# Kernel optimization log

Hardware: AMD Instinct MI355X
Metric: run time of the kernel (lower is better)

## Reference

```python
import jax, jax.numpy as jnp
import numpy as np

B, C, H, W = 512, 3, 32, 32
N = 50000
D = C * H * W  # 3072


def setup_inputs() -> dict:
    key = jax.random.key(0)
    k1, k2, k3 = jax.random.split(key, 3)
    x = jax.random.normal(k1, (B, C, H, W), dtype=jnp.float32)
    # per-sample noise levels, strictly positive
    sigma = jax.random.uniform(k2, (B,), dtype=jnp.float32, minval=0.5, maxval=2.0)
    # reference dataset, normalized images in [-1, 1], flattened to (N, D)
    y = jax.random.uniform(k3, (N, D), dtype=jnp.float32, minval=-1.0, maxval=1.0)
    return {"x": x, "sigma": sigma, "y": y}


def reference(x, sigma, y):
    Bb, Cc, Hh, Ww = x.shape
    xf = x.astype(jnp.float32).reshape(Bb, Cc * Hh * Ww)          # (B, D)
    s = sigma.astype(jnp.float32).reshape(-1, 1)                  # (B, 1)
    # squared euclidean distance via the GEMM expansion (matches cdist(p=2)**2)
    x2 = jnp.sum(xf * xf, axis=1, keepdims=True)                  # (B, 1)
    y2 = jnp.sum(y * y, axis=1)[None, :]                          # (1, N)
    d2 = jnp.maximum(x2 + y2 - 2.0 * (xf @ y.T), 0.0)             # (B, N)
    logits = -d2 / (2.0 * s * s)                                  # (B, N)
    prob = jax.nn.softmax(logits, axis=1)                         # (B, N)
    denoised = prob @ y                                           # (B, D)
    return denoised.reshape(Bb, Cc, Hh, Ww)
```

## Files before the change

### kernel.cpp

```cpp
#include <hip/hip_runtime.h>


typedef __attribute__((ext_vector_type(4))) float f32x4;
typedef __attribute__((ext_vector_type(4))) int i32x4;
typedef __attribute__((ext_vector_type(4))) char c8x4;
typedef __attribute__((ext_vector_type(16))) char c8x16;
typedef __attribute__((ext_vector_type(4))) unsigned short u16x4;
typedef __attribute__((ext_vector_type(8))) unsigned short u16x8;
typedef __attribute__((ext_vector_type(8))) __bf16 bf16x8;

#define NREAL 50000
#define NP    50176
#define DD    3072
#define BB    512

#define WAIT0  asm volatile("s_waitcnt vmcnt(0)" ::: "memory")
#define VM2    asm volatile("s_waitcnt vmcnt(2)" ::: "memory")
#define VM6    asm volatile("s_waitcnt vmcnt(6)" ::: "memory")
#define VM10   asm volatile("s_waitcnt vmcnt(10)" ::: "memory")
#define LGKM0  asm volatile("s_waitcnt lgkmcnt(0)" ::: "memory")
#define BAR    __builtin_amdgcn_s_barrier()
#define SCHED0 __builtin_amdgcn_sched_barrier(0)

#define SX (6.0f / 127.0f)
#define SY (1.0f / 127.0f)

__device__ __forceinline__ unsigned short f32_bf16_rne(float f) {
  unsigned int u = __float_as_uint(f);
  unsigned int r = 0x7FFFu + ((u >> 16) & 1u);
  return (unsigned short)((u + r) >> 16);
}
__device__ __forceinline__ void gload16(const void* g, void* l) {
  __builtin_amdgcn_global_load_lds(
      (const __attribute__((address_space(1))) void*)g,
      (__attribute__((address_space(3))) void*)l, 16, 0, 0);
}
__device__ __forceinline__ bf16x8 ldsldb(const unsigned short* p) {
  return __builtin_bit_cast(bf16x8, *(const u16x8*)p);
}
__device__ __forceinline__ i32x4 ldsld4(const char* p) {
  return *(const i32x4*)p;
}
__device__ __forceinline__ char q8(float f, float sc) {
  float an = rintf(f * sc);
  an = fminf(127.f, fmaxf(-127.f, an));
  return (char)(int)an;
}

__global__ __launch_bounds__(256) void zero_kernel(f32x4* p) {
  p[(size_t)blockIdx.x * 256 + threadIdx.x] = (f32x4){0.f, 0.f, 0.f, 0.f};
}

__global__ __launch_bounds__(256) void init_kernel(int* rowmin, float* rowsum) {
  const int i = blockIdx.x * 256 + threadIdx.x;
  if (i < BB) { rowmin[i] = 0x7F800000; rowsum[i] = 0.f; }
}

__global__ __launch_bounds__(256) void prep_x_kernel(
    const float* __restrict__ x, const float* __restrict__ sigma,
    char* __restrict__ ax, char* __restrict__ bx,
    float* __restrict__ x2, float* __restrict__ inv2s2) {
  const int b = blockIdx.x, t = threadIdx.x;
  const f32x4* xr = (const f32x4*)(x + (size_t)b * DD);
  float ssq = 0.f;
#pragma unroll
  for (int i = 0; i < 3; ++i) {
    const int idx = i * 256 + t;
    f32x4 v = xr[idx];
    c8x4 a, bb;
#pragma unroll
    for (int j = 0; j < 4; ++j) {
      float f = v[j];
      ssq += f * f;
      char av = q8(f, 127.0f / 6.0f);
      a[j] = av;
      float r = f - (float)(int)av * SX;
      bb[j] = q8(r, 254.0f * 127.0f / 6.0f);
    }
    *(c8x4*)(ax + (size_t)b * DD + idx * 4) = a;
    *(c8x4*)(bx + (size_t)b * DD + idx * 4) = bb;
  }
  __shared__ float red[4];
#pragma unroll
  for (int off = 32; off > 0; off >>= 1) ssq += __shfl_xor(ssq, off);
  if ((t & 63) == 0) red[t >> 6] = ssq;
  __syncthreads();
  if (t == 0) {
    x2[b] = red[0] + red[1] + red[2] + red[3];
    float s = sigma[b];
    inv2s2[b] = 1.0f / (2.0f * s * s);
  }
}

__global__ __launch_bounds__(256) void quant_y_kernel(
    const float* __restrict__ y, char* __restrict__ ay, char* __restrict__ by,
    float* __restrict__ y2) {
  const int n = blockIdx.x, t = threadIdx.x;
  if (n >= NREAL) {
    c8x4 z = {0, 0, 0, 0};
#pragma unroll
    for (int i = 0; i < 3; ++i) {
      const int idx = i * 256 + t;
      *(c8x4*)(ay + (size_t)n * DD + idx * 4) = z;
      *(c8x4*)(by + (size_t)n * DD + idx * 4) = z;
    }
    if (t == 0) y2[n] = 0.f;
    return;
  }
  const f32x4* yr = (const f32x4*)(y + (size_t)n * DD);
  float ssq = 0.f;
#pragma unroll
  for (int i = 0; i < 3; ++i) {
    const int idx = i * 256 + t;
    f32x4 v = yr[idx];
    c8x4 a, bb;
#pragma unroll
    for (int j = 0; j < 4; ++j) {
      float f = v[j];
      ssq += f * f;
      char av = q8(f, 127.0f);
      a[j] = av;
      float r2 = f - (float)(int)av * SY;
      bb[j] = q8(r2, 254.0f * 127.0f);
    }
    *(c8x4*)(ay + (size_t)n * DD + idx * 4) = a;
    *(c8x4*)(by + (size_t)n * DD + idx * 4) = bb;
  }
  __shared__ float red[4];
#pragma unroll
  for (int off = 32; off > 0; off >>= 1) ssq += __shfl_xor(ssq, off);
  if ((t & 63) == 0) red[t >> 6] = ssq;
  __syncthreads();
  if (t == 0) y2[n] = red[0] + red[1] + red[2] + red[3];
}

__global__ __launch_bounds__(256) void tr_y_kernel(
    const char* __restrict__ ay, const char* __restrict__ by,
    unsigned short* __restrict__ yT) {
  const int bn = blockIdx.x % 784, bd = blockIdx.x / 784;
  const int n0 = bn * 64, d0 = bd * 64;
  __shared__ unsigned short T[64][66];
  const int t = threadIdx.x;
  const int r = t >> 2, cc = (t & 3) * 16;
  c8x16 a = *(const c8x16*)(ay + (size_t)(n0 + r) * DD + d0 + cc);
  c8x16 b = *(const c8x16*)(by + (size_t)(n0 + r) * DD + d0 + cc);
#pragma unroll
  for (int j = 0; j < 16; ++j) {
    float f = (float)((int)a[j] * 254 + (int)b[j]) * (SY / 254.0f);
    T[r][cc + j] = f32_bf16_rne(f);
  }
  __syncthreads();
  const int dr = t >> 2;
#pragma unroll
  for (int k = 0; k < 2; ++k) {
    const int nb = ((t & 3) * 2 + k) * 8;
    u16x8 o;
#pragma unroll
    for (int j = 0; j < 8; ++j) o[j] = T[nb + j][dr];
    *(u16x8*)(yT + (size_t)(d0 + dr) * NP + n0 + nb) = o;
  }
}

__global__ __launch_bounds__(512, 2) void qk_kernel(
    const char* __restrict__ ay, const char* __restrict__ by,
    const char* __restrict__ ax, const char* __restrict__ bx,
    const float* __restrict__ x2, const float* __restrict__ inv2s2,
    const float* __restrict__ y2, float* __restrict__ S, int* __restrict__ rowmin) {
  const int orig = blockIdx.x;
  const int virt = (orig & 7) * 98 + (orig >> 3);
  const int mt = virt & 1, nt = virt >> 1;
  const int m0 = mt * 256, n0 = nt * 128;
  const int t = threadIdx.x, lane = t & 63, w = t >> 6;
  const int wm = w >> 1, wn = w & 1;
  const int l15 = lane & 15;
  const int cs = ((lane >> 4) ^ ((l15 >> 1) & 3)) * 16;

  __shared__ __align__(16) char L[3][49152];

  i32x4 acc1[4][4] = {};
  i32x4 acc2[4][4] = {};

  const int srow = t >> 2;
  const int sc = ((t & 3) ^ ((t >> 3) & 3)) * 16;
  const int sdst = t * 16;

  const char* pax0 = ax + (size_t)(m0 + srow) * DD + sc;
  const char* pax1 = ax + (size_t)(m0 + srow + 128) * DD + sc;
  const char* pbx0 = bx + (size_t)(m0 + srow) * DD + sc;
  const char* pbx1 = bx + (size_t)(m0 + srow + 128) * DD + sc;
  const char* pay = ay + (size_t)(n0 + srow) * DD + sc;
  const char* pby = by + (size_t)(n0 + srow) * DD + sc;

  auto SA = [&](int buf) {
    char* base = L[buf];
    gload16(pax0, base + sdst);
    gload16(pax1, base + 8192 + sdst);
    gload16(pbx0, base + 16384 + sdst);
    gload16(pbx1, base + 16384 + 8192 + sdst);
    pax0 += 64; pax1 += 64; pbx0 += 64; pbx1 += 64;
  };
  auto SB = [&](int buf) {
    char* base = L[buf];
    gload16(pay, base + 32768 + sdst);
    gload16(pby, base + 40960 + sdst);
    pay += 64; pby += 64;
  };

  i32x4 ayf[4], byf[4], axf[2], bxf[2];
  auto RB = [&](int buf) {
    const char* base = L[buf];
#pragma unroll
    for (int nf = 0; nf < 4; ++nf) {
      const int row = wn * 64 + nf * 16 + l15;
      ayf[nf] = ldsld4(base + 32768 + row * 64 + cs);
      byf[nf] = ldsld4(base + 40960 + row * 64 + cs);
    }
  };
  auto RA = [&](int buf, int mh) {
    const char* base = L[buf];
#pragma unroll
    for (int m2 = 0; m2 < 2; ++m2) {
      const int row = wm * 64 + (mh * 2 + m2) * 16 + l15;
      axf[m2] = ldsld4(base + row * 64 + cs);
      bxf[m2] = ldsld4(base + 16384 + row * 64 + cs);
    }
  };
  auto MF = [&](int mh) {
    __builtin_amdgcn_s_setprio(1);
#pragma unroll
    for (int m2 = 0; m2 < 2; ++m2) {
      const int mf = mh * 2 + m2;
#pragma unroll
      for (int nf = 0; nf < 4; ++nf) {
        acc1[mf][nf] = __builtin_amdgcn_mfma_i32_16x16x64_i8(axf[m2], ayf[nf], acc1[mf][nf], 0, 0, 0);
        acc2[mf][nf] = __builtin_amdgcn_mfma_i32_16x16x64_i8(axf[m2], byf[nf], acc2[mf][nf], 0, 0, 0);
        acc2[mf][nf] = __builtin_amdgcn_mfma_i32_16x16x64_i8(bxf[m2], ayf[nf], acc2[mf][nf], 0, 0, 0);
      }
    }
    __builtin_amdgcn_s_setprio(0);
  };

  SA(0); SB(0); SA(1); SB(1);

  for (int k = 0; k < 48; ++k) {
    const int buf = k % 3;
    BAR;
    if (k <= 45) SA((k + 2) % 3);
    if (k <= 45) { VM10; } else if (k == 46) { VM6; } else { WAIT0; }
    BAR;
    RB(buf); RA(buf, 0);
    MF(0);
    if (k <= 45) SB((k + 2) % 3);
    RA(buf, 1);
    MF(1);
  }

  const float C1 = 6.0f / 16129.0f;
  const float C2 = C1 / 254.0f;
  float rmv[4][4];
#pragma unroll
  for (int mf = 0; mf < 4; ++mf)
#pragma unroll
    for (int i = 0; i < 4; ++i) rmv[mf][i] = 3.0e38f;

#pragma unroll
  for (int nf = 0; nf < 4; ++nf) {
    const int col = n0 + wn * 64 + nf * 16 + l15;
    const bool ok = (col < NREAL);
    const float yy = ok ? y2[col] : 0.f;
#pragma unroll
    for (int mf = 0; mf < 4; ++mf) {
#pragma unroll
      for (int i = 0; i < 4; ++i) {
        const int row = m0 + wm * 64 + mf * 16 + ((lane >> 4) * 4) + i;
        float v = 3.0e38f;
        if (ok) {
          float dot = C1 * (float)acc1[mf][nf][i] + C2 * (float)acc2[mf][nf][i];
          float d2 = fmaxf(x2[row] + yy - 2.0f * dot, 0.0f);
          v = d2 * inv2s2[row];
          rmv[mf][i] = fminf(rmv[mf][i], v);
        }
        S[(size_t)row * NP + col] = v;
      }
    }
  }
#pragma unroll
  for (int mf = 0; mf < 4; ++mf)
#pragma unroll
    for (int i = 0; i < 4; ++i) {
      float v = rmv[mf][i];
#pragma unroll
      for (int o = 1; o < 16; o <<= 1) v = fminf(v, __shfl_xor(v, o));
      rmv[mf][i] = v;
    }
  if (l15 == 0) {
#pragma unroll
    for (int mf = 0; mf < 4; ++mf)
#pragma unroll
      for (int i = 0; i < 4; ++i) {
        const int row = m0 + wm * 64 + mf * 16 + ((lane >> 4) * 4) + i;
        atomicMin(rowmin + row, __float_as_int(rmv[mf][i]));
      }
  }
}

__global__ __launch_bounds__(256) void softmax_kernel(
    const float* __restrict__ S, const int* __restrict__ rowmin,
    unsigned short* __restrict__ P, float* __restrict__ rowsum) {
  const int bid = blockIdx.x;
  const int b = bid / 7, c = bid % 7;
  const int t = threadIdx.x;
  const f32x4* row = (const f32x4*)(S + (size_t)b * NP);
  const float rm = __int_as_float(rowmin[b]);
  unsigned short* pr = P + (size_t)b * NP;
  float sum = 0.f;
  const int base = c * 1792;
#pragma unroll
  for (int i = 0; i < 7; ++i) {
    const int e = base + i * 256 + t;
    f32x4 v = row[e];
    float e0 = __expf(rm - v[0]), e1 = __expf(rm - v[1]);
    float e2 = __expf(rm - v[2]), e3 = __expf(rm - v[3]);
    sum += e0 + e1 + e2 + e3;
    u16x4 o;
    o[0] = f32_bf16_rne(e0); o[1] = f32_bf16_rne(e1);
    o[2] = f32_bf16_rne(e2); o[3] = f32_bf16_rne(e3);
    *(u16x4*)(pr + (size_t)e * 4) = o;
  }
#pragma unroll
  for (int off = 32; off > 0; off >>= 1) sum += __shfl_xor(sum, off);
  __shared__ float red[4];
  if ((t & 63) == 0) red[t >> 6] = sum;
  __syncthreads();
  if (t == 0) atomicAdd(rowsum + b, red[0] + red[1] + red[2] + red[3]);
}

__global__ __launch_bounds__(512, 2) void pv_kernel(
    const unsigned short* __restrict__ yT, const unsigned short* __restrict__ P,
    const float* __restrict__ rowsum, float* __restrict__ out) {
  const int orig = blockIdx.x;
  const int virt = (orig & 7) * 96 + (orig >> 3);
  const int sp = virt / 24;
  const int r24 = virt % 24;
  const int dt = r24 >> 1, mt = r24 & 1;
  const int m0 = mt * 256, d0 = dt * 256;
  const int k0t = sp * 24 + (sp < 16 ? sp : 16);
  const int NT = 24 + (sp < 16 ? 1 : 0);

  const int t = threadIdx.x;
  const int lane = t & 63, w = t >> 6;
  const int wm = w >> 2, wn = w & 3;
  const int l15 = lane & 15;
  const int h3 = (l15 >> 1) & 7;
  const int cs0 = ((lane >> 4) ^ h3) * 8;
  const int cs1 = ((4 + (lane >> 4)) ^ h3) * 8;

  __shared__ __align__(16) unsigned short L[2][2][16384];

  f32x4 acc[8][4] = {};

  const int srow8 = t >> 3;
  const int sc = ((t & 7) ^ ((t >> 4) & 7)) * 8;
  const int sdst = t * 8;

  const size_t kbeg = (size_t)k0t * 64;
  const unsigned short* pA[4];
  pA[0] = P + (size_t)(m0 + srow8) * NP + kbeg + sc;
  pA[1] = P + (size_t)(m0 + srow8 + 128) * NP + kbeg + sc;
  pA[2] = P + (size_t)(m0 + srow8 + 64) * NP + kbeg + sc;
  pA[3] = P + (size_t)(m0 + srow8 + 192) * NP + kbeg + sc;
  const unsigned short* pB[4];
#pragma unroll
  for (int r = 0; r < 4; ++r)
    pB[r] = yT + (size_t)(d0 + srow8 + r * 64) * NP + kbeg + sc;

  auto SB01 = [&](int b) {
    gload16(pB[0], &L[b][1][sdst]); gload16(pB[1], &L[b][1][sdst + 4096]);
    pB[0] += 64; pB[1] += 64;
  };
  auto SB23 = [&](int b) {
    gload16(pB[2], &L[b][1][sdst + 8192]); gload16(pB[3], &L[b][1][sdst + 12288]);
    pB[2] += 64; pB[3] += 64;
  };
  auto SA01 = [&](int b) {
    gload16(pA[0], &L[b][0][sdst]); gload16(pA[1], &L[b][0][sdst + 4096]);
    pA[0] += 64; pA[1] += 64;
  };
  auto SA23 = [&](int b) {
    gload16(pA[2], &L[b][0][sdst + 8192]); gload16(pA[3], &L[b][0][sdst + 12288]);
    pA[2] += 64; pA[3] += 64;
  };

  bf16x8 a[4], bv[4];
  auto RA = [&](int b, int mh, int cs) {
#pragma unroll
    for (int m4 = 0; m4 < 4; ++m4)
      a[m4] = ldsldb(&L[b][0][(mh * 128 + wm * 64 + m4 * 16 + l15) * 64 + cs]);
  };
  auto RB = [&](int b, int cs) {
#pragma unroll
    for (int nf = 0; nf < 4; ++nf)
      bv[nf] = ldsldb(&L[b][1][(wn * 64 + nf * 16 + l15) * 64 + cs]);
  };
  auto MF = [&](int mh) {
    __builtin_amdgcn_s_setprio(1);
#pragma unroll
    for (int m4 = 0; m4 < 4; ++m4)
#pragma unroll
      for (int nf = 0; nf < 4; ++nf)
        acc[mh * 4 + m4][nf] = __builtin_amdgcn_mfma_f32_16x16x32_bf16(
            a[m4], bv[nf], acc[mh * 4 + m4][nf], 0, 0, 0);
    __builtin_amdgcn_s_setprio(0);
  };

  SB01(0); SB23(0); SA01(0); SA23(0);
  WAIT0; BAR;

  for (int k = 0; k < NT - 1; ++k) {
    const int b = k & 1, nb = b ^ 1;
    RB(b, cs0); RA(b, 0, cs0);
    SB01(nb);
    BAR; LGKM0; SCHED0;
    MF(0);
    VM2;
    BAR;
    RA(b, 1, cs0);
    SB23(nb);
    BAR; LGKM0; SCHED0;
    MF(1);
    BAR;
    RB(b, cs1); RA(b, 0, cs1);
    SA01(nb);
    BAR; LGKM0; SCHED0;
    MF(0);
    BAR;
    RA(b, 1, cs1);
    SA23(nb);
    BAR; LGKM0; SCHED0;
    MF(1);
    VM2;
    BAR;
  }
  {
    const int b = (NT - 1) & 1;
    RB(b, cs0); RA(b, 0, cs0);
    BAR; LGKM0; SCHED0;
    MF(0);
    WAIT0;
    BAR;
    RA(b, 1, cs0);
    LGKM0; SCHED0;
    MF(1);
    RB(b, cs1); RA(b, 0, cs1);
    LGKM0; SCHED0;
    MF(0);
    RA(b, 1, cs1);
    LGKM0; SCHED0;
    MF(1);
  }

#pragma unroll
  for (int mi = 0; mi < 8; ++mi)
#pragma unroll
    for (int i = 0; i < 4; ++i) {
      const int row = m0 + wm * 128 + mi * 16 + ((lane >> 4) * 4) + i;
      const float scale = 1.0f / rowsum[row];
#pragma unroll
      for (int nf = 0; nf < 4; ++nf) {
        const int col = d0 + wn * 64 + nf * 16 + l15;
        unsafeAtomicAdd(out + (size_t)row * DD + col, acc[mi][nf][i] * scale);
      }
    }
}

extern "C" void kernel_launch(void* const* d_in, const int* in_sizes, int n_in,
                              void* d_out, int out_size, void* d_ws, size_t ws_size,
                              hipStream_t stream) {
  const float* x = (const float*)d_in[0];
  const float* sigma = (const float*)d_in[1];
  const float* y = (const float*)d_in[2];
  float* out = (float*)d_out;
  char* ws = (char*)d_ws;

  size_t off = 0;
  float* S = (float*)(ws + off);                      off += (size_t)BB * NP * 4;
  char* ay = (char*)(ws + off);                       off += (size_t)NP * DD;
  char* by = (char*)(ws + off);                       off += (size_t)NP * DD;
  unsigned short* P = (unsigned short*)by;
  char* ax = (char*)(ws + off);                       off += (size_t)BB * DD;
  char* bx = (char*)(ws + off);                       off += (size_t)BB * DD;
  float* y2 = (float*)(ws + off);                     off += (size_t)NP * 4;
  float* x2 = (float*)(ws + off);                     off += 512 * 4;
  float* inv2s2 = (float*)(ws + off);                 off += 512 * 4;
  float* rowsum = (float*)(ws + off);                 off += 512 * 4;
  int* rowmin = (int*)(ws + off);                     off += 512 * 4;
  unsigned short* yT = (unsigned short*)(ws + off);   off += (size_t)DD * NP * 2;
  off += 65536;
  if (ws_size < off) return;

  zero_kernel<<<dim3(1536), dim3(256), 0, stream>>>((f32x4*)out);
  init_kernel<<<dim3(2), dim3(256), 0, stream>>>(rowmin, rowsum);
  prep_x_kernel<<<dim3(512), dim3(256), 0, stream>>>(x, sigma, ax, bx, x2, inv2s2);
  quant_y_kernel<<<dim3(NP), dim3(256), 0, stream>>>(y, ay, by, y2);
  tr_y_kernel<<<dim3(784 * 48), dim3(256), 0, stream>>>(ay, by, yT);
  qk_kernel<<<dim3(784), dim3(512), 0, stream>>>(ay, by, ax, bx, x2, inv2s2, y2, S, rowmin);
  softmax_kernel<<<dim3(512 * 7), dim3(256), 0, stream>>>(S, rowmin, P, rowsum);
  pv_kernel<<<dim3(768), dim3(512), 0, stream>>>(yT, P, rowsum, out);
}
```

Before: 931.4 us.

## Shrink QK GEMM tiles to 128x128 with single-buffered LDS staging

The int8 distance GEMM now uses 256-thread blocks computing 128x128 output tiles, so twice as many blocks are launched. The triple-buffered, barrier-interleaved global→LDS pipeline is replaced by one 32KB buffer filled between two __syncthreads per k-step. The intent is to cut LDS use and raise occupancy and block count. In exchange, load latency no longer overlaps with MFMA work, and operand reuse per byte loaded drops.

```diff
diff --git a/kernel.cpp b/kernel.cpp
--- a/kernel.cpp
+++ b/kernel.cpp
@@ -16,8 +16,6 @@
 
 #define WAIT0  asm volatile("s_waitcnt vmcnt(0)" ::: "memory")
 #define VM2    asm volatile("s_waitcnt vmcnt(2)" ::: "memory")
-#define VM6    asm volatile("s_waitcnt vmcnt(6)" ::: "memory")
-#define VM10   asm volatile("s_waitcnt vmcnt(10)" ::: "memory")
 #define LGKM0  asm volatile("s_waitcnt lgkmcnt(0)" ::: "memory")
 #define BAR    __builtin_amdgcn_s_barrier()
 #define SCHED0 __builtin_amdgcn_sched_barrier(0)
@@ -161,21 +159,21 @@
   }
 }
 
-__global__ __launch_bounds__(512, 2) void qk_kernel(
+__global__ __launch_bounds__(256, 2) void qk_kernel(
     const char* __restrict__ ay, const char* __restrict__ by,
     const char* __restrict__ ax, const char* __restrict__ bx,
     const float* __restrict__ x2, const float* __restrict__ inv2s2,
     const float* __restrict__ y2, float* __restrict__ S, int* __restrict__ rowmin) {
   const int orig = blockIdx.x;
-  const int virt = (orig & 7) * 98 + (orig >> 3);
-  const int mt = virt & 1, nt = virt >> 1;
-  const int m0 = mt * 256, n0 = nt * 128;
+  const int virt = (orig & 7) * 196 + (orig >> 3);
+  const int mt = virt & 3, nt = virt >> 2;
+  const int m0 = mt * 128, n0 = nt * 128;
   const int t = threadIdx.x, lane = t & 63, w = t >> 6;
   const int wm = w >> 1, wn = w & 1;
   const int l15 = lane & 15;
   const int cs = ((lane >> 4) ^ ((l15 >> 1) & 3)) * 16;
 
-  __shared__ __align__(16) char L[3][49152];
+  __shared__ __align__(16) char L[32768];
 
   i32x4 acc1[4][4] = {};
   i32x4 acc2[4][4] = {};
@@ -185,74 +183,58 @@
   const int sdst = t * 16;
 
   const char* pax0 = ax + (size_t)(m0 + srow) * DD + sc;
-  const char* pax1 = ax + (size_t)(m0 + srow + 128) * DD + sc;
+  const char* pax1 = ax + (size_t)(m0 + srow + 64) * DD + sc;
   const char* pbx0 = bx + (size_t)(m0 + srow) * DD + sc;
-  const char* pbx1 = bx + (size_t)(m0 + srow + 128) * DD + sc;
-  const char* pay = ay + (size_t)(n0 + srow) * DD + sc;
-  const char* pby = by + (size_t)(n0 + srow) * DD + sc;
-
-  auto SA = [&](int buf) {
-    char* base = L[buf];
-    gload16(pax0, base + sdst);
-    gload16(pax1, base + 8192 + sdst);
-    gload16(pbx0, base + 16384 + sdst);
-    gload16(pbx1, base + 16384 + 8192 + sdst);
+  const char* pbx1 = bx + (size_t)(m0 + srow + 64) * DD + sc;
+  const char* pay0 = ay + (size_t)(n0 + srow) * DD + sc;
+  const char* pay1 = ay + (size_t)(n0 + srow + 64) * DD + sc;
+  const char* pby0 = by + (size_t)(n0 + srow) * DD + sc;
+  const char* pby1 = by + (size_t)(n0 + srow + 64) * DD + sc;
+
+  auto STAGE = [&]() {
+    gload16(pax0, L + sdst);
+    gload16(pax1, L + 4096 + sdst);
+    gload16(pbx0, L + 8192 + sdst);
+    gload16(pbx1, L + 12288 + sdst);
+    gload16(pay0, L + 16384 + sdst);
+    gload16(pay1, L + 20480 + sdst);
+    gload16(pby0, L + 24576 + sdst);
+    gload16(pby1, L + 28672 + sdst);
     pax0 += 64; pax1 += 64; pbx0 += 64; pbx1 += 64;
-  };
-  auto SB = [&](int buf) {
-    char* base = L[buf];
-    gload16(pay, base + 32768 + sdst);
-    gload16(pby, base + 40960 + sdst);
-    pay += 64; pby += 64;
-  };
-
-  i32x4 ayf[4], byf[4], axf[2], bxf[2];
-  auto RB = [&](int buf) {
-    const char* base = L[buf];
+    pay0 += 64; pay1 += 64; pby0 += 64; pby1 += 64;
+  };
+  auto COMPUTE = [&]() {
+    i32x4 axf[4], bxf[4], ayf[4], byf[4];
 #pragma unroll
     for (int nf = 0; nf < 4; ++nf) {
       const int row = wn * 64 + nf * 16 + l15;
-      ayf[nf] = ldsld4(base + 32768 + row * 64 + cs);
-      byf[nf] = ldsld4(base + 40960 + row * 64 + cs);
-    }
-  };
-  auto RA = [&](int buf, int mh) {
-    const char* base = L[buf];
-#pragma unroll
-    for (int m2 = 0; m2 < 2; ++m2) {
-      const int row = wm * 64 + (mh * 2 + m2) * 16 + l15;
-      axf[m2] = ldsld4(base + row * 64 + cs);
-      bxf[m2] = ldsld4(base + 16384 + row * 64 + cs);
-    }
-  };
-  auto MF = [&](int mh) {
+      ayf[nf] = ldsld4(L + 16384 + row * 64 + cs);
+      byf[nf] = ldsld4(L + 24576 + row * 64 + cs);
+    }
+#pragma unroll
+    for (int mf = 0; mf < 4; ++mf) {
+      const int row = wm * 64 + mf * 16 + l15;
+      axf[mf] = ldsld4(L + row * 64 + cs);
+      bxf[mf] = ldsld4(L + 8192 + row * 64 + cs);
+    }
     __builtin_amdgcn_s_setprio(1);
 #pragma unroll
-    for (int m2 = 0; m2 < 2; ++m2) {
-      const int mf = mh * 2 + m2;
+    for (int mf = 0; mf < 4; ++mf)
 #pragma unroll
       for (int nf = 0; nf < 4; ++nf) {
-        acc1[mf][nf] = __builtin_amdgcn_mfma_i32_16x16x64_i8(axf[m2], ayf[nf], acc1[mf][nf], 0, 0, 0);
-        acc2[mf][nf] = __builtin_amdgcn_mfma_i32_16x16x64_i8(axf[m2], byf[nf], acc2[mf][nf], 0, 0, 0);
-        acc2[mf][nf] = __builtin_amdgcn_mfma_i32_16x16x64_i8(bxf[m2], ayf[nf], acc2[mf][nf], 0, 0, 0);
+        acc1[mf][nf] = __builtin_amdgcn_mfma_i32_16x16x64_i8(axf[mf], ayf[nf], acc1[mf][nf], 0, 0, 0);
+        acc2[mf][nf] = __builtin_amdgcn_mfma_i32_16x16x64_i8(axf[mf], byf[nf], acc2[mf][nf], 0, 0, 0);
+        acc2[mf][nf] = __builtin_amdgcn_mfma_i32_16x16x64_i8(bxf[mf], ayf[nf], acc2[mf][nf], 0, 0, 0);
       }
-    }
     __builtin_amdgcn_s_setprio(0);
   };
 
-  SA(0); SB(0); SA(1); SB(1);
-
+  STAGE();
   for (int k = 0; k < 48; ++k) {
-    const int buf = k % 3;
-    BAR;
-    if (k <= 45) SA((k + 2) % 3);
-    if (k <= 45) { VM10; } else if (k == 46) { VM6; } else { WAIT0; }
-    BAR;
-    RB(buf); RA(buf, 0);
-    MF(0);
-    if (k <= 45) SB((k + 2) % 3);
-    RA(buf, 1);
-    MF(1);
+    __syncthreads();
+    COMPUTE();
+    __syncthreads();
+    if (k < 47) STAGE();
   }
 
   const float C1 = 6.0f / 16129.0f;
@@ -503,7 +485,7 @@
   prep_x_kernel<<<dim3(512), dim3(256), 0, stream>>>(x, sigma, ax, bx, x2, inv2s2);
   quant_y_kernel<<<dim3(NP), dim3(256), 0, stream>>>(y, ay, by, y2);
   tr_y_kernel<<<dim3(784 * 48), dim3(256), 0, stream>>>(ay, by, yT);
-  qk_kernel<<<dim3(784), dim3(512), 0, stream>>>(ay, by, ax, bx, x2, inv2s2, y2, S, rowmin);
+  qk_kernel<<<dim3(1568), dim3(256), 0, stream>>>(ay, by, ax, bx, x2, inv2s2, y2, S, rowmin);
   softmax_kernel<<<dim3(512 * 7), dim3(256), 0, stream>>>(S, rowmin, P, rowsum);
   pv_kernel<<<dim3(768), dim3(512), 0, stream>>>(yT, P, rowsum, out);
 }
```

Measured after the change: 921.7 us. About the same (-1.1%).
